# Optimization experiments

Hardware: AMD Instinct MI355X
Metric: run time of the kernel (lower is better)

Reference implementation:

```python
import jax, jax.numpy as jnp
import numpy as np

H = 64            # hidden_dim
N_NODES = 100000
N_EDGES = 2000000
IN_DIM = 2 * H + 2  # src_emb || dst_emb || src_fiedler || dst_fiedler


def setup_inputs() -> dict:
    key = jax.random.key(0)
    ks = jax.random.split(key, 10)
    node_embeddings = jax.random.normal(ks[0], (N_NODES, H), dtype=jnp.float32)
    edge_index = jax.random.randint(ks[1], (2, N_EDGES), 0, N_NODES, dtype=jnp.int64)
    fiedler_vector = jax.random.normal(ks[2], (N_NODES,), dtype=jnp.float32)
    # MLP scorer params: Linear(130,64)+ReLU, Linear(64,64)+ReLU, Linear(64,1)
    def lin(k, fan_in, fan_out):
        bound = 1.0 / np.sqrt(fan_in)
        kw, kb = jax.random.split(k)
        W = jax.random.uniform(kw, (fan_in, fan_out), jnp.float32, -bound, bound)
        b = jax.random.uniform(kb, (fan_out,), jnp.float32, -bound, bound)
        return W, b
    W1, b1 = lin(ks[3], IN_DIM, H)
    W2, b2 = lin(ks[4], H, H)
    W3, b3 = lin(ks[5], H, 1)
    return {
        "node_embeddings": node_embeddings,
        "fiedler_vector": fiedler_vector,
        "W1": W1, "b1": b1, "W2": W2, "b2": b2, "W3": W3, "b3": b3,
        "edge_index": edge_index,
        "num_nodes": N_NODES,
    }


def reference(node_embeddings, fiedler_vector, W1, b1, W2, b2, W3, b3, edge_index, num_nodes):
    src, dst = edge_index[0], edge_index[1]
    # Gather + concat edge features: [E, 2H+2]
    feats = jnp.concatenate(
        [
            node_embeddings[src],               # [E, H]
            node_embeddings[dst],               # [E, H]
            fiedler_vector[src][:, None],        # [E, 1]
            fiedler_vector[dst][:, None],        # [E, 1]
        ],
        axis=-1,
    )
    # Edge scorer MLP (Dropout is identity in eval mode)
    h = jax.nn.relu(feats @ W1 + b1)
    h = jax.nn.relu(h @ W2 + b2)
    edge_scores = (h @ W3 + b3)[:, 0]  # [E]
    return edge_scores
```

## Files before the change

kernel.cpp:

```cpp
#include <hip/hip_runtime.h>


#define HD 64

typedef __attribute__((ext_vector_type(8))) _Float16 half8;
typedef __attribute__((ext_vector_type(4))) _Float16 half4;
typedef __attribute__((ext_vector_type(8))) short  short8;
typedef __attribute__((ext_vector_type(8))) float  float8;
typedef __attribute__((ext_vector_type(4))) float  f32x4;

__device__ __forceinline__ half8 relu_h8(half8 x) {
    short8 b = __builtin_bit_cast(short8, x);
    short8 m = b >> 15;
    b = b & ~m;
    return __builtin_bit_cast(half8, b);
}

__global__ __launch_bounds__(256) void precompute_uv(
    const float* __restrict__ emb, const float* __restrict__ fied,
    const float* __restrict__ W1, const float* __restrict__ b1,
    _Float16* __restrict__ u, _Float16* __restrict__ v,
    int n_nodes, int ntiles)
{
    const int lane = threadIdx.x & 63;
    const int q = lane >> 4;
    const int c = lane & 15;
    const int wid = blockIdx.x * (blockDim.x >> 6) + (threadIdx.x >> 6);
    const int nw  = gridDim.x * (blockDim.x >> 6);

    half8 Au[4][2], Av[4][2];
    #pragma unroll
    for (int t = 0; t < 4; ++t)
        #pragma unroll
        for (int ks = 0; ks < 2; ++ks)
            #pragma unroll
            for (int j = 0; j < 8; ++j) {
                int k = ks * 32 + q * 8 + j;
                Au[t][ks][j] = (_Float16)W1[k * HD + t * 16 + c];
                Av[t][ks][j] = (_Float16)W1[(64 + k) * HD + t * 16 + c];
            }
    f32x4 b1q[4], wsq[4], wdq[4];
    #pragma unroll
    for (int t = 0; t < 4; ++t) {
        b1q[t] = *(const f32x4*)(b1 + t * 16 + q * 4);
        wsq[t] = *(const f32x4*)(W1 + 128 * HD + t * 16 + q * 4);
        wdq[t] = *(const f32x4*)(W1 + 129 * HD + t * 16 + q * 4);
    }

    for (int tile = wid; tile < ntiles; tile += nw) {
        const int n0 = tile * 16;
        const int n  = n0 + c;
        int na = n; if (na >= n_nodes) na = n_nodes - 1;
        const float* rp = emb + (size_t)na * HD + q * 8;
        float8 a0 = *(const float8*)rp;
        float8 a1 = *(const float8*)(rp + 32);
        half8 B0 = __builtin_convertvector(a0, half8);
        half8 B1 = __builtin_convertvector(a1, half8);

        f32x4 aU[4] = {}, aV[4] = {};
        #pragma unroll
        for (int t = 0; t < 4; ++t) {
            aU[t] = __builtin_amdgcn_mfma_f32_16x16x32_f16(Au[t][0], B0, aU[t], 0, 0, 0);
            aU[t] = __builtin_amdgcn_mfma_f32_16x16x32_f16(Au[t][1], B1, aU[t], 0, 0, 0);
            aV[t] = __builtin_amdgcn_mfma_f32_16x16x32_f16(Av[t][0], B0, aV[t], 0, 0, 0);
            aV[t] = __builtin_amdgcn_mfma_f32_16x16x32_f16(Av[t][1], B1, aV[t], 0, 0, 0);
        }

        const float fv = fied[na];
        const bool ok = (n < n_nodes);
        #pragma unroll
        for (int t = 0; t < 4; ++t) {
            half4 hu, hv;
            #pragma unroll
            for (int r = 0; r < 4; ++r) {
                hu[r] = (_Float16)(aU[t][r] + b1q[t][r] + fv * wsq[t][r]);
                hv[r] = (_Float16)(aV[t][r] + fv * wdq[t][r]);
            }
            if (ok) {
                *(half4*)(u + (size_t)n * HD + t * 16 + q * 4) = hu;
                *(half4*)(v + (size_t)n * HD + t * 16 + q * 4) = hv;
            }
        }
    }
}

__global__ __launch_bounds__(256) void edge_mlp(
    const _Float16* __restrict__ u, const _Float16* __restrict__ v,
    const int* __restrict__ src, const int* __restrict__ dst,
    const float* __restrict__ W2, const float* __restrict__ b2,
    const float* __restrict__ W3, const float* __restrict__ b3,
    float* __restrict__ out, int E, int ntiles)
{
    const int lane = threadIdx.x & 63;
    const int q = lane >> 4;
    const int c = lane & 15;
    const int wid = blockIdx.x * (blockDim.x >> 6) + (threadIdx.x >> 6);
    const int nw  = gridDim.x * (blockDim.x >> 6);

    half8 Af[4][2];
    #pragma unroll
    for (int t = 0; t < 4; ++t)
        #pragma unroll
        for (int ks = 0; ks < 2; ++ks)
            #pragma unroll
            for (int j = 0; j < 8; ++j) {
                int k = ks * 32 + q * 8 + j;
                Af[t][ks][j] = (_Float16)W2[k * HD + t * 16 + c];
            }
    f32x4 b2q[4], w3q[4];
    #pragma unroll
    for (int t = 0; t < 4; ++t) {
        b2q[t] = *(const f32x4*)(b2 + t * 16 + q * 4);
        w3q[t] = *(const f32x4*)(W3 + t * 16 + q * 4);
    }
    const float b3v = b3[0];

    const int stride = nw * 2;
    const int base0  = wid * 2;

    auto eid = [&](int tile) {
        int t = tile; if (t >= ntiles) t = ntiles - 1;
        int e = t * 16 + c; if (e >= E) e = E - 1;
        return e;
    };
    auto issue = [&](int s, int d, half8& Ua, half8& Ub, half8& Va, half8& Vb) {
        const half8* up = (const half8*)(u + (unsigned)s * HD + q * 8);
        const half8* vp = (const half8*)(v + (unsigned)d * HD + q * 8);
        Ua = up[0]; Ub = up[4]; Va = vp[0]; Vb = vp[4];
    };
    auto compute_store = [&](int tile, half8 Ua, half8 Ub, half8 Va, half8 Vb) {
        half8 B0 = relu_h8(Ua + Va);
        half8 B1 = relu_h8(Ub + Vb);
        f32x4 acc[4] = {};
        #pragma unroll
        for (int t = 0; t < 4; ++t) {
            acc[t] = __builtin_amdgcn_mfma_f32_16x16x32_f16(Af[t][0], B0, acc[t], 0, 0, 0);
            acc[t] = __builtin_amdgcn_mfma_f32_16x16x32_f16(Af[t][1], B1, acc[t], 0, 0, 0);
        }
        float p = 0.f;
        #pragma unroll
        for (int t = 0; t < 4; ++t)
            #pragma unroll
            for (int r = 0; r < 4; ++r)
                p = fmaf(fmaxf(acc[t][r] + b2q[t][r], 0.f), w3q[t][r], p);
        p += __shfl_xor(p, 16, 64);
        p += __shfl_xor(p, 32, 64);
        if (q == 0) {
            int e = tile * 16 + c;
            if (e < E) out[e] = p + b3v;
        }
    };

    if (base0 >= ntiles) return;

    int e0 = eid(base0), e1 = eid(base0 + 1);
    int s0 = src[e0], d0 = dst[e0];
    int s1 = src[e1], d1 = dst[e1];
    half8 U0a, U0b, V0a, V0b, U1a, U1b, V1a, V1b;
    issue(s0, d0, U0a, U0b, V0a, V0b);
    issue(s1, d1, U1a, U1b, V1a, V1b);
    int e2 = eid(base0 + stride), e3 = eid(base0 + stride + 1);
    int sc0 = src[e2], dc0 = dst[e2];
    int sc1 = src[e3], dc1 = dst[e3];

    for (int base = base0; base < ntiles; base += stride) {
        const int f0 = eid(base + 2 * stride), f1 = eid(base + 2 * stride + 1);
        const int sn0 = src[f0], dn0 = dst[f0];
        const int sn1 = src[f1], dn1 = dst[f1];

        compute_store(base, U0a, U0b, V0a, V0b);
        issue(sc0, dc0, U0a, U0b, V0a, V0b);

        compute_store(base + 1, U1a, U1b, V1a, V1b);
        issue(sc1, dc1, U1a, U1b, V1a, V1b);

        sc0 = sn0; dc0 = dn0; sc1 = sn1; dc1 = dn1;
    }
}

extern "C" void kernel_launch(void* const* d_in, const int* in_sizes, int n_in,
                              void* d_out, int out_size, void* d_ws, size_t ws_size,
                              hipStream_t stream) {
    const float* emb  = (const float*)d_in[0];
    const float* fied = (const float*)d_in[1];
    const float* W1   = (const float*)d_in[2];
    const float* b1   = (const float*)d_in[3];
    const float* W2   = (const float*)d_in[4];
    const float* b2   = (const float*)d_in[5];
    const float* W3   = (const float*)d_in[6];
    const float* b3   = (const float*)d_in[7];
    const int*   eidx = (const int*)d_in[8];

    const int n_nodes = in_sizes[1];
    const int E       = in_sizes[8] / 2;
    const int* srcp = eidx;
    const int* dstp = eidx + E;

    _Float16* u = (_Float16*)d_ws;
    _Float16* v = u + (size_t)n_nodes * HD;

    const int ntilesN = (n_nodes + 15) / 16;
    precompute_uv<<<1024, 256, 0, stream>>>(emb, fied, W1, b1, u, v,
                                            n_nodes, ntilesN);

    const int ntilesE = (E + 15) / 16;
    edge_mlp<<<2048, 256, 0, stream>>>(u, v, srcp, dstp, W2, b2, W3, b3,
                                       (float*)d_out, E, ntilesE);
}
```

Measured before the change: 176.4 us.

## Move W2 fragments to LDS, fp16 epilogue, triple-buffer edge gathers

Result: slower. 187.1 us (+6.1%).

```diff
diff --git a/kernel.cpp b/kernel.cpp
--- a/kernel.cpp
+++ b/kernel.cpp
@@ -5,7 +5,9 @@
 
 typedef __attribute__((ext_vector_type(8))) _Float16 half8;
 typedef __attribute__((ext_vector_type(4))) _Float16 half4;
+typedef __attribute__((ext_vector_type(2))) _Float16 half2v;
 typedef __attribute__((ext_vector_type(8))) short  short8;
+typedef __attribute__((ext_vector_type(2))) short  short2v;
 typedef __attribute__((ext_vector_type(8))) float  float8;
 typedef __attribute__((ext_vector_type(4))) float  f32x4;
 
@@ -14,6 +16,15 @@
     short8 m = b >> 15;
     b = b & ~m;
     return __builtin_bit_cast(half8, b);
+}
+__device__ __forceinline__ half2v relu_h2(half2v x) {
+    short2v b = __builtin_bit_cast(short2v, x);
+    short2v m = b >> 15;
+    b = b & ~m;
+    return __builtin_bit_cast(half2v, b);
+}
+__device__ __forceinline__ half2v pkrtz(float a, float b) {
+    return __builtin_bit_cast(half2v, __builtin_amdgcn_cvt_pkrtz(a, b));
 }
 
 __global__ __launch_bounds__(256) void precompute_uv(
@@ -91,32 +102,37 @@
     const float* __restrict__ W3, const float* __restrict__ b3,
     float* __restrict__ out, int E, int ntiles)
 {
-    const int lane = threadIdx.x & 63;
+    const int tid  = threadIdx.x;
+    const int lane = tid & 63;
     const int q = lane >> 4;
     const int c = lane & 15;
-    const int wid = blockIdx.x * (blockDim.x >> 6) + (threadIdx.x >> 6);
+    const int wid = blockIdx.x * (blockDim.x >> 6) + (tid >> 6);
     const int nw  = gridDim.x * (blockDim.x >> 6);
 
-    half8 Af[4][2];
-    #pragma unroll
-    for (int t = 0; t < 4; ++t)
-        #pragma unroll
-        for (int ks = 0; ks < 2; ++ks)
-            #pragma unroll
-            for (int j = 0; j < 8; ++j) {
-                int k = ks * 32 + q * 8 + j;
-                Af[t][ks][j] = (_Float16)W2[k * HD + t * 16 + c];
-            }
-    f32x4 b2q[4], w3q[4];
+    __shared__ half8 AfL[4][2][64];
+    for (int i = tid; i < 512; i += 256) {
+        const int t = i >> 7, ks = (i >> 6) & 1, qc = i & 63;
+        const int qq = qc >> 4, cc = qc & 15;
+        half8 val;
+        #pragma unroll
+        for (int j = 0; j < 8; ++j) {
+            int k = ks * 32 + qq * 8 + j;
+            val[j] = (_Float16)W2[k * HD + t * 16 + cc];
+        }
+        AfL[t][ks][qc] = val;
+    }
+    __syncthreads();
+
+    half2v b2p[4][2], w3p[4][2];
     #pragma unroll
     for (int t = 0; t < 4; ++t) {
-        b2q[t] = *(const f32x4*)(b2 + t * 16 + q * 4);
-        w3q[t] = *(const f32x4*)(W3 + t * 16 + q * 4);
+        int f = t * 16 + q * 4;
+        b2p[t][0] = half2v{(_Float16)b2[f],     (_Float16)b2[f + 1]};
+        b2p[t][1] = half2v{(_Float16)b2[f + 2], (_Float16)b2[f + 3]};
+        w3p[t][0] = half2v{(_Float16)W3[f],     (_Float16)W3[f + 1]};
+        w3p[t][1] = half2v{(_Float16)W3[f + 2], (_Float16)W3[f + 3]};
     }
     const float b3v = b3[0];
-
-    const int stride = nw * 2;
-    const int base0  = wid * 2;
 
     auto eid = [&](int tile) {
         int t = tile; if (t >= ntiles) t = ntiles - 1;
@@ -131,18 +147,23 @@
     auto compute_store = [&](int tile, half8 Ua, half8 Ub, half8 Va, half8 Vb) {
         half8 B0 = relu_h8(Ua + Va);
         half8 B1 = relu_h8(Ub + Vb);
-        f32x4 acc[4] = {};
+        unsigned qc = (unsigned)(q * 16 + c);
+        asm("" : "+v"(qc));
+        float p = 0.f;
         #pragma unroll
         for (int t = 0; t < 4; ++t) {
-            acc[t] = __builtin_amdgcn_mfma_f32_16x16x32_f16(Af[t][0], B0, acc[t], 0, 0, 0);
-            acc[t] = __builtin_amdgcn_mfma_f32_16x16x32_f16(Af[t][1], B1, acc[t], 0, 0, 0);
-        }
-        float p = 0.f;
-        #pragma unroll
-        for (int t = 0; t < 4; ++t)
-            #pragma unroll
-            for (int r = 0; r < 4; ++r)
-                p = fmaf(fmaxf(acc[t][r] + b2q[t][r], 0.f), w3q[t][r], p);
+            f32x4 acc = {};
+            acc = __builtin_amdgcn_mfma_f32_16x16x32_f16(AfL[t][0][qc], B0, acc, 0, 0, 0);
+            acc = __builtin_amdgcn_mfma_f32_16x16x32_f16(AfL[t][1][qc], B1, acc, 0, 0, 0);
+            half2v h0 = pkrtz(acc[0], acc[1]);
+            half2v h1 = pkrtz(acc[2], acc[3]);
+            h0 = relu_h2(h0 + b2p[t][0]);
+            h1 = relu_h2(h1 + b2p[t][1]);
+            p = __builtin_amdgcn_fdot2(__builtin_bit_cast(__fp16 __attribute__((ext_vector_type(2))), h0),
+                                       __builtin_bit_cast(__fp16 __attribute__((ext_vector_type(2))), w3p[t][0]), p, false);
+            p = __builtin_amdgcn_fdot2(__builtin_bit_cast(__fp16 __attribute__((ext_vector_type(2))), h1),
+                                       __builtin_bit_cast(__fp16 __attribute__((ext_vector_type(2))), w3p[t][1]), p, false);
+        }
         p += __shfl_xor(p, 16, 64);
         p += __shfl_xor(p, 32, 64);
         if (q == 0) {
@@ -151,30 +172,38 @@
         }
     };
 
+    const int stride = nw * 3;
+    const int base0  = wid * 3;
     if (base0 >= ntiles) return;
 
-    int e0 = eid(base0), e1 = eid(base0 + 1);
+    int e0 = eid(base0), e1 = eid(base0 + 1), e2 = eid(base0 + 2);
     int s0 = src[e0], d0 = dst[e0];
     int s1 = src[e1], d1 = dst[e1];
-    half8 U0a, U0b, V0a, V0b, U1a, U1b, V1a, V1b;
+    int s2 = src[e2], d2 = dst[e2];
+    half8 U0a, U0b, V0a, V0b, U1a, U1b, V1a, V1b, U2a, U2b, V2a, V2b;
     issue(s0, d0, U0a, U0b, V0a, V0b);
     issue(s1, d1, U1a, U1b, V1a, V1b);
-    int e2 = eid(base0 + stride), e3 = eid(base0 + stride + 1);
-    int sc0 = src[e2], dc0 = dst[e2];
-    int sc1 = src[e3], dc1 = dst[e3];
+    issue(s2, d2, U2a, U2b, V2a, V2b);
+    int f0 = eid(base0 + stride), f1 = eid(base0 + stride + 1), f2 = eid(base0 + stride + 2);
+    int sc0 = src[f0], dc0 = dst[f0];
+    int sc1 = src[f1], dc1 = dst[f1];
+    int sc2 = src[f2], dc2 = dst[f2];
 
     for (int base = base0; base < ntiles; base += stride) {
-        const int f0 = eid(base + 2 * stride), f1 = eid(base + 2 * stride + 1);
-        const int sn0 = src[f0], dn0 = dst[f0];
-        const int sn1 = src[f1], dn1 = dst[f1];
-
-        compute_store(base, U0a, U0b, V0a, V0b);
+        const int g0 = eid(base + 2 * stride), g1 = eid(base + 2 * stride + 1),
+                  g2 = eid(base + 2 * stride + 2);
+        const int sn0 = src[g0], dn0 = dst[g0];
+        const int sn1 = src[g1], dn1 = dst[g1];
+        const int sn2 = src[g2], dn2 = dst[g2];
+
+        compute_store(base,     U0a, U0b, V0a, V0b);
         issue(sc0, dc0, U0a, U0b, V0a, V0b);
-
         compute_store(base + 1, U1a, U1b, V1a, V1b);
         issue(sc1, dc1, U1a, U1b, V1a, V1b);
-
-        sc0 = sn0; dc0 = dn0; sc1 = sn1; dc1 = dn1;
+        compute_store(base + 2, U2a, U2b, V2a, V2b);
+        issue(sc2, dc2, U2a, U2b, V2a, V2b);
+
+        sc0 = sn0; dc0 = dn0; sc1 = sn1; dc1 = dn1; sc2 = sn2; dc2 = dn2;
     }
 }
 
@@ -204,6 +233,6 @@
                                             n_nodes, ntilesN);
 
     const int ntilesE = (E + 15) / 16;
-    edge_mlp<<<2048, 256, 0, stream>>>(u, v, srcp, dstp, W2, b2, W3, b3,
+    edge_mlp<<<4096, 256, 0, stream>>>(u, v, srcp, dstp, W2, b2, W3, b3,
                                        (float*)d_out, E, ntilesE);
 }
```

## Deepen edge gather pipeline to four tiles and use packed fp16 epilogue

Applied to the files above, without the earlier changes.

New measurement: 183.7 us. 1.04x slower.

```diff
diff --git a/kernel.cpp b/kernel.cpp
--- a/kernel.cpp
+++ b/kernel.cpp
@@ -5,7 +5,10 @@
 
 typedef __attribute__((ext_vector_type(8))) _Float16 half8;
 typedef __attribute__((ext_vector_type(4))) _Float16 half4;
+typedef __attribute__((ext_vector_type(2))) _Float16 half2v;
+typedef __attribute__((ext_vector_type(2))) __fp16  fp16x2;
 typedef __attribute__((ext_vector_type(8))) short  short8;
+typedef __attribute__((ext_vector_type(2))) short  short2v;
 typedef __attribute__((ext_vector_type(8))) float  float8;
 typedef __attribute__((ext_vector_type(4))) float  f32x4;
 
@@ -14,6 +17,19 @@
     short8 m = b >> 15;
     b = b & ~m;
     return __builtin_bit_cast(half8, b);
+}
+__device__ __forceinline__ half2v relu_h2(half2v x) {
+    short2v b = __builtin_bit_cast(short2v, x);
+    short2v m = b >> 15;
+    b = b & ~m;
+    return __builtin_bit_cast(half2v, b);
+}
+__device__ __forceinline__ half2v pkrtz(float a, float b) {
+    return __builtin_bit_cast(half2v, __builtin_amdgcn_cvt_pkrtz(a, b));
+}
+__device__ __forceinline__ float fdot2f(half2v a, half2v b, float c) {
+    return __builtin_amdgcn_fdot2(__builtin_bit_cast(fp16x2, a),
+                                  __builtin_bit_cast(fp16x2, b), c, false);
 }
 
 __global__ __launch_bounds__(256) void precompute_uv(
@@ -107,16 +123,16 @@
                 int k = ks * 32 + q * 8 + j;
                 Af[t][ks][j] = (_Float16)W2[k * HD + t * 16 + c];
             }
-    f32x4 b2q[4], w3q[4];
+    half2v b2p[4][2], w3p[4][2];
     #pragma unroll
     for (int t = 0; t < 4; ++t) {
-        b2q[t] = *(const f32x4*)(b2 + t * 16 + q * 4);
-        w3q[t] = *(const f32x4*)(W3 + t * 16 + q * 4);
+        int f = t * 16 + q * 4;
+        b2p[t][0] = half2v{(_Float16)b2[f],     (_Float16)b2[f + 1]};
+        b2p[t][1] = half2v{(_Float16)b2[f + 2], (_Float16)b2[f + 3]};
+        w3p[t][0] = half2v{(_Float16)W3[f],     (_Float16)W3[f + 1]};
+        w3p[t][1] = half2v{(_Float16)W3[f + 2], (_Float16)W3[f + 3]};
     }
     const float b3v = b3[0];
-
-    const int stride = nw * 2;
-    const int base0  = wid * 2;
 
     auto eid = [&](int tile) {
         int t = tile; if (t >= ntiles) t = ntiles - 1;
@@ -131,18 +147,17 @@
     auto compute_store = [&](int tile, half8 Ua, half8 Ub, half8 Va, half8 Vb) {
         half8 B0 = relu_h8(Ua + Va);
         half8 B1 = relu_h8(Ub + Vb);
-        f32x4 acc[4] = {};
+        float p = 0.f;
         #pragma unroll
         for (int t = 0; t < 4; ++t) {
-            acc[t] = __builtin_amdgcn_mfma_f32_16x16x32_f16(Af[t][0], B0, acc[t], 0, 0, 0);
-            acc[t] = __builtin_amdgcn_mfma_f32_16x16x32_f16(Af[t][1], B1, acc[t], 0, 0, 0);
-        }
-        float p = 0.f;
-        #pragma unroll
-        for (int t = 0; t < 4; ++t)
-            #pragma unroll
-            for (int r = 0; r < 4; ++r)
-                p = fmaf(fmaxf(acc[t][r] + b2q[t][r], 0.f), w3q[t][r], p);
+            f32x4 acc = {};
+            acc = __builtin_amdgcn_mfma_f32_16x16x32_f16(Af[t][0], B0, acc, 0, 0, 0);
+            acc = __builtin_amdgcn_mfma_f32_16x16x32_f16(Af[t][1], B1, acc, 0, 0, 0);
+            half2v h0 = relu_h2(pkrtz(acc[0], acc[1]) + b2p[t][0]);
+            half2v h1 = relu_h2(pkrtz(acc[2], acc[3]) + b2p[t][1]);
+            p = fdot2f(h0, w3p[t][0], p);
+            p = fdot2f(h1, w3p[t][1], p);
+        }
         p += __shfl_xor(p, 16, 64);
         p += __shfl_xor(p, 32, 64);
         if (q == 0) {
@@ -151,30 +166,45 @@
         }
     };
 
+    const int stride = nw * 4;
+    const int base0  = wid * 4;
     if (base0 >= ntiles) return;
 
-    int e0 = eid(base0), e1 = eid(base0 + 1);
-    int s0 = src[e0], d0 = dst[e0];
-    int s1 = src[e1], d1 = dst[e1];
-    half8 U0a, U0b, V0a, V0b, U1a, U1b, V1a, V1b;
-    issue(s0, d0, U0a, U0b, V0a, V0b);
-    issue(s1, d1, U1a, U1b, V1a, V1b);
-    int e2 = eid(base0 + stride), e3 = eid(base0 + stride + 1);
-    int sc0 = src[e2], dc0 = dst[e2];
-    int sc1 = src[e3], dc1 = dst[e3];
+    half8 U0a,U0b,V0a,V0b, U1a,U1b,V1a,V1b, U2a,U2b,V2a,V2b, U3a,U3b,V3a,V3b;
+    {
+        int e0 = eid(base0), e1 = eid(base0+1), e2 = eid(base0+2), e3 = eid(base0+3);
+        issue(src[e0], dst[e0], U0a, U0b, V0a, V0b);
+        issue(src[e1], dst[e1], U1a, U1b, V1a, V1b);
+        issue(src[e2], dst[e2], U2a, U2b, V2a, V2b);
+        issue(src[e3], dst[e3], U3a, U3b, V3a, V3b);
+    }
+    int sc0, dc0, sc1, dc1, sc2, dc2, sc3, dc3;
+    {
+        int f0 = eid(base0+stride),   f1 = eid(base0+stride+1),
+            f2 = eid(base0+stride+2), f3 = eid(base0+stride+3);
+        sc0 = src[f0]; dc0 = dst[f0]; sc1 = src[f1]; dc1 = dst[f1];
+        sc2 = src[f2]; dc2 = dst[f2]; sc3 = src[f3]; dc3 = dst[f3];
+    }
 
     for (int base = base0; base < ntiles; base += stride) {
-        const int f0 = eid(base + 2 * stride), f1 = eid(base + 2 * stride + 1);
-        const int sn0 = src[f0], dn0 = dst[f0];
-        const int sn1 = src[f1], dn1 = dst[f1];
-
-        compute_store(base, U0a, U0b, V0a, V0b);
+        const int g0 = eid(base + 2*stride),     g1 = eid(base + 2*stride + 1),
+                  g2 = eid(base + 2*stride + 2), g3 = eid(base + 2*stride + 3);
+        const int sn0 = src[g0], dn0 = dst[g0];
+        const int sn1 = src[g1], dn1 = dst[g1];
+        const int sn2 = src[g2], dn2 = dst[g2];
+        const int sn3 = src[g3], dn3 = dst[g3];
+
+        compute_store(base,     U0a, U0b, V0a, V0b);
         issue(sc0, dc0, U0a, U0b, V0a, V0b);
-
         compute_store(base + 1, U1a, U1b, V1a, V1b);
         issue(sc1, dc1, U1a, U1b, V1a, V1b);
+        compute_store(base + 2, U2a, U2b, V2a, V2b);
+        issue(sc2, dc2, U2a, U2b, V2a, V2b);
+        compute_store(base + 3, U3a, U3b, V3a, V3b);
+        issue(sc3, dc3, U3a, U3b, V3a, V3b);
 
         sc0 = sn0; dc0 = dn0; sc1 = sn1; dc1 = dn1;
+        sc2 = sn2; dc2 = dn2; sc3 = sn3; dc3 = dn3;
     }
 }
 
```
